# Kernel optimization log

Hardware: AMD Instinct MI355X
Metric: run time of the kernel (lower is better)

## Reference

```python
import jax, jax.numpy as jnp
import numpy as np

N_NODES = 50000
N_EDGES = 1600000
F_NODE = 8
F_EDGE = 4
HIDDEN = 16
OUT = 8
MLP_HID = 25


def _nnconv(x, src, dst, edge_attr, wa, ba, wb, bb, root, bias, out_ch):
    # edge MLP -> per-edge weight matrix [E, in_ch, out_ch]
    h = jax.nn.relu(edge_attr @ wa + ba) @ wb + bb
    w = h.reshape(-1, x.shape[1], out_ch)
    # gather source node feats, per-edge small matmul
    msg = jnp.einsum('ei,eio->eo', x[src], w)  # [E, out_ch]
    n = x.shape[0]
    agg = jax.ops.segment_sum(msg, dst, num_segments=n)
    cnt = jax.ops.segment_sum(jnp.ones((msg.shape[0],), msg.dtype), dst, num_segments=n)
    agg = agg / jnp.maximum(cnt, 1.0)[:, None]  # mean aggregation
    return agg + x @ root + bias  # root weight + bias (PyG NNConv defaults)


def setup_inputs() -> dict:
    key = jax.random.key(0)
    ks = jax.random.split(key, 16)
    s = lambda k, shape, fan: jax.random.normal(k, shape, jnp.float32) * (1.0 / np.sqrt(fan))
    return {
        'x': jax.random.normal(ks[0], (N_NODES, F_NODE), jnp.float32),
        'edge_index': jax.random.randint(ks[1], (2, N_EDGES), 0, N_NODES),
        'edge_attr': jax.random.normal(ks[2], (N_EDGES, F_EDGE), jnp.float32),
        # conv1 edge-MLP: F_EDGE -> 25 -> F_NODE*HIDDEN
        'w1a': s(ks[3], (F_EDGE, MLP_HID), F_EDGE), 'b1a': jnp.zeros((MLP_HID,), jnp.float32),
        'w1b': s(ks[4], (MLP_HID, F_NODE * HIDDEN), MLP_HID), 'b1b': jnp.zeros((F_NODE * HIDDEN,), jnp.float32),
        'root1': s(ks[5], (F_NODE, HIDDEN), F_NODE), 'bias1': jnp.zeros((HIDDEN,), jnp.float32),
        # conv2 edge-MLP: F_EDGE -> 25 -> HIDDEN*OUT
        'w2a': s(ks[6], (F_EDGE, MLP_HID), F_EDGE), 'b2a': jnp.zeros((MLP_HID,), jnp.float32),
        'w2b': s(ks[7], (MLP_HID, HIDDEN * OUT), MLP_HID), 'b2b': jnp.zeros((HIDDEN * OUT,), jnp.float32),
        'root2': s(ks[8], (HIDDEN, OUT), HIDDEN), 'bias2': jnp.zeros((OUT,), jnp.float32),
    }


def reference(x, edge_index, edge_attr, w1a, b1a, w1b, b1b, root1, bias1,
              w2a, b2a, w2b, b2b, root2, bias2):
    src, dst = edge_index[0], edge_index[1]
    h = _nnconv(x, src, dst, edge_attr, w1a, b1a, w1b, b1b, root1, bias1, HIDDEN)
    h = jax.nn.relu(h)
    # dropout p=0.5 is identity in eval mode
    out = _nnconv(h, src, dst, edge_attr, w2a, b2a, w2b, b2b, root2, bias2, OUT)
    return out
```

## Files before the change

### kernel.cpp

```cpp
#include <hip/hip_runtime.h>
#include <hip/hip_fp16.h>

#define NN 50000
#define NE 1600000
#define FN 8
#define FE 4
#define HID 16
#define OC 8
#define MH 25
#define CAP 80
#define BINS 196
#define BCAP 8960
#define TILE 4096


typedef int iv4 __attribute__((ext_vector_type(4)));
static __device__ __forceinline__ int4 ntload4(const int4* p) {
    iv4 v = __builtin_nontemporal_load(reinterpret_cast<const iv4*>(p));
    return make_int4(v.x, v.y, v.z, v.w);
}
static __device__ __forceinline__ unsigned pack2h(float lo, float hi) {
    return ((unsigned)__half_as_ushort(__float2half_rn(hi)) << 16)
         |  (unsigned)__half_as_ushort(__float2half_rn(lo));
}

#define PKFMA_LO(acc, a, b) \
    asm("v_pk_fma_f16 %0, %1, %2, %0 op_sel:[0,0,0] op_sel_hi:[0,1,1]" \
        : "+v"(acc) : "v"(a), "v"(b))
#define PKFMA_HI(acc, a, b) \
    asm("v_pk_fma_f16 %0, %1, %2, %0 op_sel:[1,0,0] op_sel_hi:[1,1,1]" \
        : "+v"(acc) : "v"(a), "v"(b))
#define PKMAX0(dst, a) \
    asm("v_pk_max_f16 %0, %1, 0" : "=v"(dst) : "v"(a))

static __device__ __forceinline__ void unpack2(unsigned u, float& lo, float& hi) {
    __half2 h; *reinterpret_cast<unsigned*>(&h) = u;
    float2 f = __half22float2(h);
    lo = f.x; hi = f.y;
}

__global__ void __launch_bounds__(256) xhalf_kernel(const float4* __restrict__ x4,
                                                    uint4* __restrict__ xh4) {
    int n = blockIdx.x * 256 + threadIdx.x;
    if (n < NN) {
        float4 a = x4[2 * n], b = x4[2 * n + 1];
        xh4[n] = make_uint4(pack2h(a.x, a.y), pack2h(a.z, a.w),
                            pack2h(b.x, b.y), pack2h(b.z, b.w));
    }
}

__global__ void __launch_bounds__(512) binA_kernel(
    const int* __restrict__ ei, const float* __restrict__ ea,
    unsigned* __restrict__ gcursor, int4* __restrict__ binbuf) {
    __shared__ unsigned hist[256], lstart[256], run[256], basei[256];
    __shared__ unsigned scanbuf[256];
    __shared__ int4 stage[TILE];
    for (int t = threadIdx.x; t < 256; t += 512) { hist[t] = 0u; run[t] = 0u; }
    __syncthreads();

    const int bb = blockIdx.x * TILE;
    const int tid = threadIdx.x;
    int dsts[8], srcs[8];
    bool actk[2];
#pragma unroll
    for (int k = 0; k < 2; ++k) {
        int e = bb + k * 2048 + tid * 4;
        actk[k] = e < NE;
        int4 d = make_int4(0, 0, 0, 0), s = make_int4(0, 0, 0, 0);
        if (actk[k]) {
            d = *reinterpret_cast<const int4*>(ei + NE + e);
            s = *reinterpret_cast<const int4*>(ei + e);
        }
        dsts[4 * k]     = d.x; dsts[4 * k + 1] = d.y;
        dsts[4 * k + 2] = d.z; dsts[4 * k + 3] = d.w;
        srcs[4 * k]     = s.x; srcs[4 * k + 1] = s.y;
        srcs[4 * k + 2] = s.z; srcs[4 * k + 3] = s.w;
        if (actk[k]) {
            atomicAdd(&hist[d.x >> 8], 1u);
            atomicAdd(&hist[d.y >> 8], 1u);
            atomicAdd(&hist[d.z >> 8], 1u);
            atomicAdd(&hist[d.w >> 8], 1u);
        }
    }
    __syncthreads();
    if (tid < 256) scanbuf[tid] = hist[tid];
    __syncthreads();
    for (int off = 1; off < 256; off <<= 1) {
        unsigned v = 0u;
        if (tid < 256 && tid >= off) v = scanbuf[tid - off];
        __syncthreads();
        if (tid < 256) scanbuf[tid] += v;
        __syncthreads();
    }
    if (tid < 256) lstart[tid] = scanbuf[tid] - hist[tid];
    if (tid < BINS) basei[tid] = hist[tid] ? atomicAdd(&gcursor[tid], hist[tid]) : 0u;
    __syncthreads();

#pragma unroll
    for (int k = 0; k < 2; ++k) {
        if (!actk[k]) continue;
        int e = bb + k * 2048 + tid * 4;
#pragma unroll
        for (int j = 0; j < 4; ++j) {
            float4 a = *reinterpret_cast<const float4*>(ea + 4ull * (e + j));
            unsigned u01 = pack2h(a.x, a.y);
            unsigned u23 = pack2h(a.z, a.w);
            int d = dsts[4 * k + j];
            int b = d >> 8;
            unsigned off = atomicAdd(&run[b], 1u);
            stage[lstart[b] + off] = make_int4(srcs[4 * k + j], d, (int)u01, (int)u23);
        }
    }
    __syncthreads();

    const int tot = (bb + TILE <= NE) ? TILE : (NE - bb);
    for (int i = tid; i < tot; i += 512) {
        int4 r = stage[i];
        int b = r.y >> 8;
        unsigned slot = basei[b] + ((unsigned)i - lstart[b]);
        if (slot < BCAP) binbuf[(size_t)b * BCAP + slot] = r;
    }
}

__global__ void __launch_bounds__(512) binB_kernel(
    const int4* __restrict__ binbuf, const unsigned* __restrict__ gcursor,
    unsigned* __restrict__ cursorF, int4* __restrict__ recs) {
    int b   = blockIdx.x >> 2;
    int sub = blockIdx.x & 3;
    unsigned cnt = gcursor[b];
    if (cnt > BCAP) cnt = BCAP;
    const int4* srcp = binbuf + (size_t)b * BCAP;
    for (unsigned i = threadIdx.x + sub * 512u; i < cnt; i += 2048u) {
        int4 r = ntload4(srcp + i);
        int dst = r.y;
        unsigned pos = atomicAdd(&cursorF[dst], 1u);
        if (pos < CAP)
            recs[(size_t)dst * CAP + pos] = make_int4(r.x, r.z, r.w, 0);
    }
}

__global__ void __launch_bounds__(512, 8) conv1_kernel(
    const float* __restrict__ x, const __half* __restrict__ xh,
    const int4* __restrict__ recs, const unsigned* __restrict__ cnts,
    const float* __restrict__ wa, const float* __restrict__ ba,
    const float* __restrict__ wb, const float* __restrict__ bb,
    const float* __restrict__ root, const float* __restrict__ bias,
    float* __restrict__ hn)
{
    __shared__ float s_wa[FE * MH];
    __shared__ float s_ba[MH];
    __shared__ float s_wb[26 * 129];
    __shared__ float s_root[FN * HID];
    __shared__ float s_bias[HID];
    __shared__ uint2 s_ea[8][4][17];
    __shared__ uint4 s_g[8][4][17];
    for (int t = threadIdx.x; t < FE * MH; t += 512) s_wa[t] = wa[t];
    for (int t = threadIdx.x; t < MH; t += 512) s_ba[t] = ba[t];
    for (int t = threadIdx.x; t < 26 * 128; t += 512) {
        int r = t >> 7, c = t & 127;
        s_wb[r * 129 + c] = (r < MH) ? wb[t] : bb[c];
    }
    for (int t = threadIdx.x; t < FN * HID; t += 512) s_root[t] = root[t];
    for (int t = threadIdx.x; t < HID; t += 512) s_bias[t] = bias[t];
    {
        float* pg = reinterpret_cast<float*>(&s_g[0][0][0]);
        for (int t = threadIdx.x; t < 8 * 4 * 17 * 4; t += 512) pg[t] = 0.f;
    }
    __syncthreads();

    const float4* x4 = reinterpret_cast<const float4*>(x);
    const int w = threadIdx.x >> 6;
    const int l = threadIdx.x & 63;
    const int q = l >> 4;
    const int m = l & 15;
    const int n = blockIdx.x * 32 + w * 4 + q;
    const unsigned cnt = (n < NN) ? cnts[n] : 0u;
    const unsigned lim = cnt < CAP ? cnt : (unsigned)CAP;
    const size_t base = (size_t)n * CAP;
    unsigned cm = lim;
    cm = max(cm, (unsigned)__shfl_xor((int)cm, 16));
    cm = max(cm, (unsigned)__shfl_xor((int)cm, 32));

    const int m2 = m + 16;
    float wB0 = 0.f, wB1 = 0.f, wB2 = 0.f, wB3 = 0.f, bB = 0.f;
    if (m2 < MH) { wB0 = s_wa[m2]; wB1 = s_wa[MH + m2]; wB2 = s_wa[2 * MH + m2];
                   wB3 = s_wa[3 * MH + m2]; bB = s_ba[m2]; }
    else if (m2 == MH) bB = 1.f;
    const unsigned wAB0 = pack2h(s_wa[m], wB0);
    const unsigned wAB1 = pack2h(s_wa[MH + m], wB1);
    const unsigned wAB2 = pack2h(s_wa[2 * MH + m], wB2);
    const unsigned wAB3 = pack2h(s_wa[3 * MH + m], wB3);
    const unsigned bAB  = pack2h(s_ba[m], bB);

    unsigned TA[4] = {0u,0u,0u,0u}, TB[4] = {0u,0u,0u,0u};
    for (unsigned c = 0; c < cm; c += 16) {
        if (c + (unsigned)m < lim) {
            int4 r = ntload4(&recs[base + c + m]);
            s_ea[w][q][m] = make_uint2((unsigned)r.y, (unsigned)r.z);
            s_g[w][q][m] = *reinterpret_cast<const uint4*>(xh + 8ull * r.x);
        }
        asm volatile("s_waitcnt lgkmcnt(0)" ::: "memory");
#pragma unroll 4
        for (int j = 0; j < 16; ++j) {
            uint2 eu = s_ea[w][q][j];
            uint4 gu = s_g[w][q][j];
            unsigned hm2 = bAB;
            PKFMA_LO(hm2, eu.x, wAB0);
            PKFMA_HI(hm2, eu.x, wAB1);
            PKFMA_LO(hm2, eu.y, wAB2);
            PKFMA_HI(hm2, eu.y, wAB3);
            PKMAX0(hm2, hm2);
            bool act = (c + (unsigned)j) < lim;
            hm2 = act ? hm2 : 0u;
            PKFMA_LO(TA[0], hm2, gu.x); PKFMA_LO(TA[1], hm2, gu.y);
            PKFMA_LO(TA[2], hm2, gu.z); PKFMA_LO(TA[3], hm2, gu.w);
            PKFMA_HI(TB[0], hm2, gu.x); PKFMA_HI(TB[1], hm2, gu.y);
            PKFMA_HI(TB[2], hm2, gu.z); PKFMA_HI(TB[3], hm2, gu.w);
        }
        asm volatile("" ::: "memory");
    }

    float T[8], U[8];
    unpack2(TA[0], T[0], T[1]); unpack2(TA[1], T[2], T[3]);
    unpack2(TA[2], T[4], T[5]); unpack2(TA[3], T[6], T[7]);
    unpack2(TB[0], U[0], U[1]); unpack2(TB[1], U[2], U[3]);
    unpack2(TB[2], U[4], U[5]); unpack2(TB[3], U[6], U[7]);

    const int rb = (m2 <= MH) ? m2 : MH;
    float s[16];
#pragma unroll
    for (int o = 0; o < 16; ++o) {
        const float* wv = s_wb + m * 129 + o;
        const float* wu = s_wb + rb * 129 + o;
        float pm = T[0]*wv[0]  + T[1]*wv[16] + T[2]*wv[32] + T[3]*wv[48]
                 + T[4]*wv[64] + T[5]*wv[80] + T[6]*wv[96] + T[7]*wv[112]
                 + U[0]*wu[0]  + U[1]*wu[16] + U[2]*wu[32] + U[3]*wu[48]
                 + U[4]*wu[64] + U[5]*wu[80] + U[6]*wu[96] + U[7]*wu[112];
        pm += __shfl_xor(pm, 8, 16);
        pm += __shfl_xor(pm, 4, 16);
        pm += __shfl_xor(pm, 2, 16);
        pm += __shfl_xor(pm, 1, 16);
        s[o] = pm;
    }

    if (m == 0 && n < NN) {
        float inv = 1.f / fmaxf((float)cnt, 1.f);
        float4 xa = x4[2 * n], xb = x4[2 * n + 1];
        float xn[8] = {xa.x, xa.y, xa.z, xa.w, xb.x, xb.y, xb.z, xb.w};
        float v[16];
#pragma unroll
        for (int o = 0; o < 16; ++o) {
            float r = s[o] * inv + s_bias[o];
#pragma unroll
            for (int i = 0; i < 8; ++i) r += xn[i] * s_root[i * HID + o];
            v[o] = fmaxf(r, 0.f);
        }
        float4* hp = reinterpret_cast<float4*>(hn + 16ull * n);
        hp[0] = make_float4(v[0], v[1], v[2], v[3]);
        hp[1] = make_float4(v[4], v[5], v[6], v[7]);
        hp[2] = make_float4(v[8], v[9], v[10], v[11]);
        hp[3] = make_float4(v[12], v[13], v[14], v[15]);
    }
}

__global__ void __launch_bounds__(256) hn2h_kernel(const float4* __restrict__ hn4,
                                                   uint4* __restrict__ hh4) {
    int n = blockIdx.x * 256 + threadIdx.x;
    if (n < NN) {
        float4 a = hn4[4 * n],     b = hn4[4 * n + 1];
        float4 c = hn4[4 * n + 2], d = hn4[4 * n + 3];
        hh4[2 * n]     = make_uint4(pack2h(a.x, a.y), pack2h(a.z, a.w),
                                    pack2h(b.x, b.y), pack2h(b.z, b.w));
        hh4[2 * n + 1] = make_uint4(pack2h(c.x, c.y), pack2h(c.z, c.w),
                                    pack2h(d.x, d.y), pack2h(d.z, d.w));
    }
}

__global__ void __launch_bounds__(512, 8) conv2_kernel(
    const __half* __restrict__ hh, const int4* __restrict__ recs,
    const unsigned* __restrict__ cnts,
    const float* __restrict__ wa, const float* __restrict__ ba,
    const float* __restrict__ wb, const float* __restrict__ bb,
    const float* __restrict__ root, const float* __restrict__ bias,
    float* __restrict__ out)
{
    __shared__ float s_wa[FE * MH];
    __shared__ float s_ba[MH];
    __shared__ float s_wb[26 * 129];
    __shared__ float s_root[HID * OC];
    __shared__ float s_bias[OC];
    __shared__ uint2 s_ea[8][4][17];
    __shared__ uint4 s_gA[8][4][17];
    __shared__ uint4 s_gB[8][4][17];
    for (int t = threadIdx.x; t < FE * MH; t += 512) s_wa[t] = wa[t];
    for (int t = threadIdx.x; t < MH; t += 512) s_ba[t] = ba[t];
    for (int t = threadIdx.x; t < 26 * 128; t += 512) {
        int r = t >> 7, c = t & 127;
        s_wb[r * 129 + c] = (r < MH) ? wb[t] : bb[c];
    }
    for (int t = threadIdx.x; t < HID * OC; t += 512) s_root[t] = root[t];
    for (int t = threadIdx.x; t < OC; t += 512) s_bias[t] = bias[t];
    {
        float* pg = reinterpret_cast<float*>(&s_gA[0][0][0]);
        for (int t = threadIdx.x; t < 8 * 4 * 17 * 4; t += 512) pg[t] = 0.f;
        float* ph = reinterpret_cast<float*>(&s_gB[0][0][0]);
        for (int t = threadIdx.x; t < 8 * 4 * 17 * 4; t += 512) ph[t] = 0.f;
    }
    __syncthreads();

    const int w = threadIdx.x >> 6;
    const int l = threadIdx.x & 63;
    const int q = l >> 4;
    const int m = l & 15;
    const int n = blockIdx.x * 32 + w * 4 + q;
    const unsigned cnt = (n < NN) ? cnts[n] : 0u;
    const unsigned lim = cnt < CAP ? cnt : (unsigned)CAP;
    const size_t base = (size_t)n * CAP;
    unsigned cm = lim;
    cm = max(cm, (unsigned)__shfl_xor((int)cm, 16));
    cm = max(cm, (unsigned)__shfl_xor((int)cm, 32));

    const int m2 = m + 16;
    float wB0 = 0.f, wB1 = 0.f, wB2 = 0.f, wB3 = 0.f, bB = 0.f;
    if (m2 < MH) { wB0 = s_wa[m2]; wB1 = s_wa[MH + m2]; wB2 = s_wa[2 * MH + m2];
                   wB3 = s_wa[3 * MH + m2]; bB = s_ba[m2]; }
    else if (m2 == MH) bB = 1.f;
    const unsigned wAB0 = pack2h(s_wa[m], wB0);
    const unsigned wAB1 = pack2h(s_wa[MH + m], wB1);
    const unsigned wAB2 = pack2h(s_wa[2 * MH + m], wB2);
    const unsigned wAB3 = pack2h(s_wa[3 * MH + m], wB3);
    const unsigned bAB  = pack2h(s_ba[m], bB);

    unsigned TA[8] = {0u,0u,0u,0u,0u,0u,0u,0u};
    unsigned TB[8] = {0u,0u,0u,0u,0u,0u,0u,0u};
    for (unsigned c = 0; c < cm; c += 16) {
        if (c + (unsigned)m < lim) {
            int4 r = ntload4(&recs[base + c + m]);
            s_ea[w][q][m] = make_uint2((unsigned)r.y, (unsigned)r.z);
            const uint4* gp = reinterpret_cast<const uint4*>(hh + 16ull * r.x);
            s_gA[w][q][m] = gp[0];
            s_gB[w][q][m] = gp[1];
        }
        asm volatile("s_waitcnt lgkmcnt(0)" ::: "memory");
#pragma unroll 4
        for (int j = 0; j < 16; ++j) {
            uint2 eu = s_ea[w][q][j];
            uint4 ga = s_gA[w][q][j];
            uint4 gb = s_gB[w][q][j];
            unsigned hm2 = bAB;
            PKFMA_LO(hm2, eu.x, wAB0);
            PKFMA_HI(hm2, eu.x, wAB1);
            PKFMA_LO(hm2, eu.y, wAB2);
            PKFMA_HI(hm2, eu.y, wAB3);
            PKMAX0(hm2, hm2);
            bool act = (c + (unsigned)j) < lim;
            hm2 = act ? hm2 : 0u;
            PKFMA_LO(TA[0], hm2, ga.x); PKFMA_LO(TA[1], hm2, ga.y);
            PKFMA_LO(TA[2], hm2, ga.z); PKFMA_LO(TA[3], hm2, ga.w);
            PKFMA_LO(TA[4], hm2, gb.x); PKFMA_LO(TA[5], hm2, gb.y);
            PKFMA_LO(TA[6], hm2, gb.z); PKFMA_LO(TA[7], hm2, gb.w);
            PKFMA_HI(TB[0], hm2, ga.x); PKFMA_HI(TB[1], hm2, ga.y);
            PKFMA_HI(TB[2], hm2, ga.z); PKFMA_HI(TB[3], hm2, ga.w);
            PKFMA_HI(TB[4], hm2, gb.x); PKFMA_HI(TB[5], hm2, gb.y);
            PKFMA_HI(TB[6], hm2, gb.z); PKFMA_HI(TB[7], hm2, gb.w);
        }
        asm volatile("" ::: "memory");
    }

    float T[16], U[16];
#pragma unroll
    for (int i = 0; i < 8; ++i) {
        unpack2(TA[i], T[2 * i], T[2 * i + 1]);
        unpack2(TB[i], U[2 * i], U[2 * i + 1]);
    }

    const int rb = (m2 <= MH) ? m2 : MH;
    float s[8];
#pragma unroll
    for (int o = 0; o < 8; ++o) {
        const float* wv = s_wb + m * 129 + o;
        const float* wu = s_wb + rb * 129 + o;
        float pm = 0.f;
#pragma unroll
        for (int i = 0; i < 16; ++i) pm += T[i] * wv[i * 8];
#pragma unroll
        for (int i = 0; i < 16; ++i) pm += U[i] * wu[i * 8];
        pm += __shfl_xor(pm, 8, 16);
        pm += __shfl_xor(pm, 4, 16);
        pm += __shfl_xor(pm, 2, 16);
        pm += __shfl_xor(pm, 1, 16);
        s[o] = pm;
    }

    if (m == 0 && n < NN) {
        float inv = 1.f / fmaxf((float)cnt, 1.f);
        uint4 ha4 = *reinterpret_cast<const uint4*>(hh + 16ull * n);
        uint4 hb4 = *reinterpret_cast<const uint4*>(hh + 16ull * n + 8);
        const __half2* ap = reinterpret_cast<const __half2*>(&ha4);
        const __half2* bp = reinterpret_cast<const __half2*>(&hb4);
        float hnn[16];
#pragma unroll
        for (int i = 0; i < 4; ++i) {
            float2 fa = __half22float2(ap[i]);
            float2 fb = __half22float2(bp[i]);
            hnn[2 * i] = fa.x; hnn[2 * i + 1] = fa.y;
            hnn[8 + 2 * i] = fb.x; hnn[8 + 2 * i + 1] = fb.y;
        }
        float v[8];
#pragma unroll
        for (int o = 0; o < 8; ++o) {
            float r = s[o] * inv + s_bias[o];
#pragma unroll
            for (int i = 0; i < 16; ++i) r += hnn[i] * s_root[i * OC + o];
            v[o] = r;
        }
        float4* op = reinterpret_cast<float4*>(out + 8ull * n);
        op[0] = make_float4(v[0], v[1], v[2], v[3]);
        op[1] = make_float4(v[4], v[5], v[6], v[7]);
    }
}

extern "C" void kernel_launch(void* const* d_in, const int* in_sizes, int n_in,
                              void* d_out, int out_size, void* d_ws, size_t ws_size,
                              hipStream_t stream) {
    const float* x     = (const float*)d_in[0];
    const int*   ei    = (const int*)d_in[1];
    const float* ea    = (const float*)d_in[2];
    const float* w1a   = (const float*)d_in[3];
    const float* b1a   = (const float*)d_in[4];
    const float* w1b   = (const float*)d_in[5];
    const float* b1b   = (const float*)d_in[6];
    const float* root1 = (const float*)d_in[7];
    const float* bias1 = (const float*)d_in[8];
    const float* w2a   = (const float*)d_in[9];
    const float* b2a   = (const float*)d_in[10];
    const float* w2b   = (const float*)d_in[11];
    const float* b2b   = (const float*)d_in[12];
    const float* root2 = (const float*)d_in[13];
    const float* bias2 = (const float*)d_in[14];
    float* out = (float*)d_out;

    char* ws = (char*)d_ws;
    int4*     recs    = (int4*)(ws);
    unsigned* cursorF = (unsigned*)(ws + 64000000);
    unsigned* gcursor = (unsigned*)(ws + 64200000);
    float*    hn      = (float*)(ws + 64200800);
    __half*   hnh     = (__half*)(ws + 67400800);
    __half*   xh      = (__half*)(ws + 69000800);
    int4*     binbuf  = (int4*)(ws + 69800800);

    hipMemsetAsync(ws + 64000000, 0, 200784, stream);
    xhalf_kernel<<<(NN + 255) / 256, 256, 0, stream>>>((const float4*)x, (uint4*)xh);
    binA_kernel<<<(NE + TILE - 1) / TILE, 512, 0, stream>>>(ei, ea, gcursor, binbuf);
    binB_kernel<<<BINS * 4, 512, 0, stream>>>(binbuf, gcursor, cursorF, recs);
    conv1_kernel<<<(NN + 31) / 32, 512, 0, stream>>>(x, xh, recs, cursorF,
                                                     w1a, b1a, w1b, b1b, root1, bias1, hn);
    hn2h_kernel<<<(NN + 255) / 256, 256, 0, stream>>>((const float4*)hn, (uint4*)hnh);
    conv2_kernel<<<(NN + 31) / 32, 512, 0, stream>>>(hnh, recs, cursorF,
                                                     w2a, b2a, w2b, b2b, root2, bias2, out);
}
```

Before: 177.7 us.

## Sort nodes by in-degree so wavefronts process similar-length edge lists

Adds a degree histogram, a prefix scan, and a scatter that build a permutation of nodes grouped by clamped in-degree. Both conv kernels then map each 16-lane group to a node through this permutation. Groups in the same wavefront get similar edge counts, so less time is lost to the max-count loop. This costs three extra small launches and a single-thread serial scan. Node accesses (recs, x, outputs) also become less contiguous.

After: 437.2 us. 2.46x slower.

```diff
diff --git a/kernel.cpp b/kernel.cpp
--- a/kernel.cpp
+++ b/kernel.cpp
@@ -139,9 +139,38 @@
     }
 }
 
+__global__ void __launch_bounds__(256) deghist_kernel(
+    const unsigned* __restrict__ cursorF, unsigned* __restrict__ deghist) {
+    int n = blockIdx.x * 256 + threadIdx.x;
+    if (n < NN) {
+        unsigned c = cursorF[n];
+        if (c > CAP) c = CAP;
+        atomicAdd(&deghist[c], 1u);
+    }
+}
+__global__ void degscan_kernel(const unsigned* __restrict__ deghist,
+                               unsigned* __restrict__ degbase) {
+    if (threadIdx.x == 0) {
+        unsigned run = 0;
+        for (int i = 0; i <= CAP; ++i) { degbase[i] = run; run += deghist[i]; }
+    }
+}
+__global__ void __launch_bounds__(256) degscatter_kernel(
+    const unsigned* __restrict__ cursorF, unsigned* __restrict__ degbase,
+    int* __restrict__ perm) {
+    int n = blockIdx.x * 256 + threadIdx.x;
+    if (n < NN) {
+        unsigned c = cursorF[n];
+        if (c > CAP) c = CAP;
+        unsigned p = atomicAdd(&degbase[c], 1u);
+        perm[p] = n;
+    }
+}
+
 __global__ void __launch_bounds__(512, 8) conv1_kernel(
     const float* __restrict__ x, const __half* __restrict__ xh,
     const int4* __restrict__ recs, const unsigned* __restrict__ cnts,
+    const int* __restrict__ perm,
     const float* __restrict__ wa, const float* __restrict__ ba,
     const float* __restrict__ wb, const float* __restrict__ bb,
     const float* __restrict__ root, const float* __restrict__ bias,
@@ -173,8 +202,10 @@
     const int l = threadIdx.x & 63;
     const int q = l >> 4;
     const int m = l & 15;
-    const int n = blockIdx.x * 32 + w * 4 + q;
-    const unsigned cnt = (n < NN) ? cnts[n] : 0u;
+    const int ni = blockIdx.x * 32 + w * 4 + q;
+    const bool valid = ni < NN;
+    const int n = valid ? perm[ni] : 0;
+    const unsigned cnt = valid ? cnts[n] : 0u;
     const unsigned lim = cnt < CAP ? cnt : (unsigned)CAP;
     const size_t base = (size_t)n * CAP;
     unsigned cm = lim;
@@ -243,7 +274,7 @@
         s[o] = pm;
     }
 
-    if (m == 0 && n < NN) {
+    if (m == 0 && valid) {
         float inv = 1.f / fmaxf((float)cnt, 1.f);
         float4 xa = x4[2 * n], xb = x4[2 * n + 1];
         float xn[8] = {xa.x, xa.y, xa.z, xa.w, xb.x, xb.y, xb.z, xb.w};
@@ -278,7 +309,7 @@
 
 __global__ void __launch_bounds__(512, 8) conv2_kernel(
     const __half* __restrict__ hh, const int4* __restrict__ recs,
-    const unsigned* __restrict__ cnts,
+    const unsigned* __restrict__ cnts, const int* __restrict__ perm,
     const float* __restrict__ wa, const float* __restrict__ ba,
     const float* __restrict__ wb, const float* __restrict__ bb,
     const float* __restrict__ root, const float* __restrict__ bias,
@@ -312,8 +343,10 @@
     const int l = threadIdx.x & 63;
     const int q = l >> 4;
     const int m = l & 15;
-    const int n = blockIdx.x * 32 + w * 4 + q;
-    const unsigned cnt = (n < NN) ? cnts[n] : 0u;
+    const int ni = blockIdx.x * 32 + w * 4 + q;
+    const bool valid = ni < NN;
+    const int n = valid ? perm[ni] : 0;
+    const unsigned cnt = valid ? cnts[n] : 0u;
     const unsigned lim = cnt < CAP ? cnt : (unsigned)CAP;
     const size_t base = (size_t)n * CAP;
     unsigned cm = lim;
@@ -392,7 +425,7 @@
         s[o] = pm;
     }
 
-    if (m == 0 && n < NN) {
+    if (m == 0 && valid) {
         float inv = 1.f / fmaxf((float)cnt, 1.f);
         uint4 ha4 = *reinterpret_cast<const uint4*>(hh + 16ull * n);
         uint4 hb4 = *reinterpret_cast<const uint4*>(hh + 16ull * n + 8);
@@ -448,14 +481,21 @@
     __half*   hnh     = (__half*)(ws + 67400800);
     __half*   xh      = (__half*)(ws + 69000800);
     int4*     binbuf  = (int4*)(ws + 69800800);
+    int*      perm    = (int*)(ws + 97899360);
+    unsigned* degbase = (unsigned*)(ws + 98099360);
+    unsigned* deghist = (unsigned*)(ws + 98099684);
 
     hipMemsetAsync(ws + 64000000, 0, 200784, stream);
+    hipMemsetAsync(ws + 98099360, 0, 648, stream);
     xhalf_kernel<<<(NN + 255) / 256, 256, 0, stream>>>((const float4*)x, (uint4*)xh);
     binA_kernel<<<(NE + TILE - 1) / TILE, 512, 0, stream>>>(ei, ea, gcursor, binbuf);
     binB_kernel<<<BINS * 4, 512, 0, stream>>>(binbuf, gcursor, cursorF, recs);
-    conv1_kernel<<<(NN + 31) / 32, 512, 0, stream>>>(x, xh, recs, cursorF,
+    deghist_kernel<<<(NN + 255) / 256, 256, 0, stream>>>(cursorF, deghist);
+    degscan_kernel<<<1, 64, 0, stream>>>(deghist, degbase);
+    degscatter_kernel<<<(NN + 255) / 256, 256, 0, stream>>>(cursorF, degbase, perm);
+    conv1_kernel<<<(NN + 31) / 32, 512, 0, stream>>>(x, xh, recs, cursorF, perm,
                                                      w1a, b1a, w1b, b1b, root1, bias1, hn);
     hn2h_kernel<<<(NN + 255) / 256, 256, 0, stream>>>((const float4*)hn, (uint4*)hnh);
-    conv2_kernel<<<(NN + 31) / 32, 512, 0, stream>>>(hnh, recs, cursorF,
+    conv2_kernel<<<(NN + 31) / 32, 512, 0, stream>>>(hnh, recs, cursorF, perm,
                                                      w2a, b2a, w2b, b2b, root2, bias2, out);
 }
```
